# Kernel tuning notes

Hardware: AMD Instinct MI355X
Metric: run time of the kernel (lower is better)

The kernel has to match this reference:

```python
import jax, jax.numpy as jnp
import numpy as np
from jax import lax

B, C, H, W = 2, 64, 384, 384
WS = 8; NH = 4; HD = C // NH; S = WS * WS  # 64 tokens per window
EPS = 1e-5


def setup_inputs() -> dict:
    key = jax.random.key(0)
    ks = jax.random.split(key, 16)
    def n(k, shape, s=0.02):
        return jax.random.normal(k, shape, jnp.float32) * s
    return {
        "x": jax.random.normal(ks[0], (B, C, H, W), jnp.float32),
        "norm1_w": jnp.ones((C,), jnp.float32), "norm1_b": jnp.zeros((C,), jnp.float32),
        "qkv_w": n(ks[1], (3 * C, C)), "qkv_b": jnp.zeros((3 * C,), jnp.float32),
        "pos_bias": n(ks[2], (1, S, NH, NH), 0.01),  # faithful: bias over (tokens, heads, heads)
        "out_w": n(ks[3], (C, C)), "out_b": jnp.zeros((C,), jnp.float32),
        "convp_w": n(ks[4], (C, C)), "convp_b": jnp.zeros((C,), jnp.float32),
        "pw1_w": n(ks[5], (C, C, 1)), "pw1_b": jnp.zeros((C,), jnp.float32),
        "dw1_w": n(ks[6], (C, 1, 3)), "dw1_b": jnp.zeros((C,), jnp.float32),
        "tok_w": n(ks[7], (C, C)), "tok_b": jnp.zeros((C,), jnp.float32),
        "norm2_w": jnp.ones((C,), jnp.float32), "norm2_b": jnp.zeros((C,), jnp.float32),
        "leff_pw_w": n(ks[8], (C, C, 1, 1)),
        "leff_dw_w": n(ks[9], (C, 1, 3, 3)), "leff_dw_b": jnp.zeros((C,), jnp.float32),
        "fc1_w": n(ks[10], (4 * C, C)), "fc1_b": jnp.zeros((4 * C,), jnp.float32),
        "fc2_w": n(ks[11], (C, 4 * C)), "fc2_b": jnp.zeros((C,), jnp.float32),
    }


def _ln_c(x, w, b):
    # channel-wise LayerNorm (Restormer 'WithBias') on (B,C,H,W), biased variance
    mu = x.mean(axis=1, keepdims=True)
    var = ((x - mu) ** 2).mean(axis=1, keepdims=True)
    return (x - mu) / jnp.sqrt(var + EPS) * w[None, :, None, None] + b[None, :, None, None]


def _lin(x, w, b):
    return x @ w.T + b


def _win_part(x):
    # (B,C,H,W) -> (B*nw, S, C); H,W divisible by WS so pad is a no-op
    b = x.shape[0]
    x = x.reshape(b, C, H // WS, WS, W // WS, WS)
    return x.transpose(0, 2, 4, 3, 5, 1).reshape(-1, S, C)


def _win_merge(wins):
    b = wins.shape[0] // ((H // WS) * (W // WS))
    x = wins.reshape(b, H // WS, W // WS, WS, WS, C)
    return x.transpose(0, 5, 1, 3, 2, 4).reshape(b, C, H, W)


def _remsa(xw, qkv_w, qkv_b, pos_bias, out_w, out_b, convp_w, convp_b,
           pw1_w, pw1_b, dw1_w, dw1_b, tok_w, tok_b):
    bw = xw.shape[0]
    qkv = _lin(xw, qkv_w, qkv_b).reshape(bw, S, NH, 3 * HD)
    q, k, v = jnp.split(qkv, 3, axis=-1)  # each (bw, S, NH, HD)
    # Faithful to source: NO head transpose -> attention mixes across the heads axis
    scores = jnp.einsum('bshd,bsgd->bshg', q, k) * (HD ** -0.5) + pos_bias  # (bw,S,NH,NH)
    attn = jax.nn.softmax(scores, axis=-1)
    ao = jnp.einsum('bshg,bsgd->bshd', attn, v).reshape(bw, S, C)
    ao = _lin(ao, out_w, out_b)
    # convolutional branch
    xc = _lin(xw, convp_w, convp_b).transpose(0, 2, 1)  # (bw, C, S)
    xc = jnp.einsum('bcs,oc->bos', xc, pw1_w[:, :, 0]) + pw1_b[None, :, None]  # 1x1 conv1d
    xc = lax.conv_general_dilated(xc, dw1_w, (1,), 'SAME', feature_group_count=C,
                                  dimension_numbers=('NCH', 'OIH', 'NCH')) + dw1_b[None, :, None]
    xc = _lin(xc.transpose(0, 2, 1), tok_w, tok_b)
    return ao + xc


def _leff(x, pw_w, dw_w, dw_b, fc1_w, fc1_b, fc2_w, fc2_b):
    b = x.shape[0]
    y = lax.conv_general_dilated(x, pw_w, (1, 1), 'SAME',
                                 dimension_numbers=('NCHW', 'OIHW', 'NCHW'))  # 1x1, no bias
    y = lax.conv_general_dilated(y, dw_w, (1, 1), 'SAME', feature_group_count=C,
                                 dimension_numbers=('NCHW', 'OIHW', 'NCHW')) + dw_b[None, :, None, None]
    y = y.transpose(0, 2, 3, 1).reshape(b, H * W, C)
    y = jax.nn.gelu(_lin(y, fc1_w, fc1_b), approximate=False)
    y = _lin(y, fc2_w, fc2_b)
    return y.reshape(b, H, W, C).transpose(0, 3, 1, 2)


def reference(x, norm1_w, norm1_b, qkv_w, qkv_b, pos_bias, out_w, out_b,
              convp_w, convp_b, pw1_w, pw1_b, dw1_w, dw1_b, tok_w, tok_b,
              norm2_w, norm2_b, leff_pw_w, leff_dw_w, leff_dw_b,
              fc1_w, fc1_b, fc2_w, fc2_b):
    xw = _win_part(_ln_c(x, norm1_w, norm1_b))
    r = _win_merge(_remsa(xw, qkv_w, qkv_b, pos_bias, out_w, out_b, convp_w, convp_b,
                          pw1_w, pw1_b, dw1_w, dw1_b, tok_w, tok_b))
    x = x + r
    x = x + _leff(_ln_c(x, norm2_w, norm2_b), leff_pw_w, leff_dw_w, leff_dw_b,
                  fc1_w, fc1_b, fc2_w, fc2_b)
    return x
```

## Files before the change

### kernel.cpp

```cpp
#include <hip/hip_runtime.h>
#include <hip/hip_bf16.h>
#include <math.h>

#define Bn 2
#define Cc 64
#define Hh 384
#define Ww 384
#define HW (Hh*Ww)
#define Tt (Bn*HW)

using f32x4  = __attribute__((ext_vector_type(4))) float;
using bf16x8 = __attribute__((ext_vector_type(8))) short;


__device__ __forceinline__ unsigned short f2bf_u(float f) {
  return __builtin_bit_cast(unsigned short, __float2bfloat16(f));
}
__device__ __forceinline__ float bf2f(unsigned short u) {
  union { unsigned u; float f; } v; v.u = ((unsigned)u) << 16;
  return v.f;
}
__device__ __forceinline__ float gelu_exact(float v) {
  return 0.5f * v * (1.0f + erff(v * 0.70710678118654752f));
}

__device__ __forceinline__ void stage_wtile(char* dst, const float* __restrict__ g, int rs, int tid) {
#pragma unroll
  for (int half = 0; half < 2; ++half) {
    int q = tid + half * 256;
    int row = q >> 3, ks = q & 7;
    const float* gp = g + (long)row * rs + ks * 8;
    float4 a = *(const float4*)gp;
    float4 b = *(const float4*)(gp + 4);
    bf16x8 o;
    o[0] = (short)f2bf_u(a.x); o[1] = (short)f2bf_u(a.y);
    o[2] = (short)f2bf_u(a.z); o[3] = (short)f2bf_u(a.w);
    o[4] = (short)f2bf_u(b.x); o[5] = (short)f2bf_u(b.y);
    o[6] = (short)f2bf_u(b.z); o[7] = (short)f2bf_u(b.w);
    *(bf16x8*)(dst + row * 128 + ((ks * 16) ^ ((row & 7) << 4))) = o;
  }
}

__device__ __forceinline__ void mfma64(const char* sA, const char* sB, int wid, int lane, f32x4 acc[4]) {
  const int r = lane & 15, kq = lane >> 4;
#pragma unroll
  for (int kh = 0; kh < 2; ++kh) {
    const int arow = wid * 16 + r;
    bf16x8 af = *(const bf16x8*)(sA + arow * 128 + ((kh * 64 + kq * 16) ^ ((arow & 7) << 4)));
#pragma unroll
    for (int nt = 0; nt < 4; ++nt) {
      const int brow = nt * 16 + r;
      bf16x8 bfv = *(const bf16x8*)(sB + brow * 128 + ((kh * 64 + kq * 16) ^ ((brow & 7) << 4)));
      acc[nt] = __builtin_amdgcn_mfma_f32_16x16x32_bf16(af, bfv, acc[nt], 0, 0, 0);
    }
  }
}


__global__ __launch_bounds__(512, 4) void kA(
    const float* __restrict__ x, unsigned short* __restrict__ x1g, unsigned short* __restrict__ yg,
    const float* __restrict__ n1w, const float* __restrict__ n1b,
    const float* __restrict__ qkvw, const float* __restrict__ qkvb,
    const float* __restrict__ posb,
    const float* __restrict__ outw, const float* __restrict__ outb,
    const float* __restrict__ cpw, const float* __restrict__ cpb,
    const float* __restrict__ pw1w, const float* __restrict__ pw1b,
    const float* __restrict__ dw1w, const float* __restrict__ dw1b,
    const float* __restrict__ tokw, const float* __restrict__ tokb,
    const float* __restrict__ n2w, const float* __restrict__ n2b,
    const float* __restrict__ lpw) {
  __shared__ char sX[16384];
  __shared__ char sW0[8192];
  __shared__ char sW1[8192];
  __shared__ char sQ[49152];

  const int tid = threadIdx.x;
  const int lane = tid & 63, wid = tid >> 6;
  const int fr = lane & 15, kq = lane >> 4;
  const int rtok = wid * 16 + fr;
  const int c0own = kq * 16;
  const int iy = wid, ix = fr;
  const int blk = blockIdx.x;
  const int b = blk / 1152;
  const int rr = blk - b * 1152;
  const int wy = rr / 24, wxp = rr - (rr / 24) * 24;
  const int h0 = wy * 8, w0 = wxp * 16;
  const long ibase = (long)b * HW;

  float4 wr0, wr1;
  const int wrow = tid >> 3, wc0 = (tid & 7) * 8;
  auto WLOAD = [&](const float* g) {
    const float* p = g + (long)wrow * 64 + wc0;
    wr0 = *(const float4*)p; wr1 = *(const float4*)(p + 4);
  };
  auto WSTORE = [&](char* dst) {
    bf16x8 o;
    o[0]=(short)f2bf_u(wr0.x); o[1]=(short)f2bf_u(wr0.y); o[2]=(short)f2bf_u(wr0.z); o[3]=(short)f2bf_u(wr0.w);
    o[4]=(short)f2bf_u(wr1.x); o[5]=(short)f2bf_u(wr1.y); o[6]=(short)f2bf_u(wr1.z); o[7]=(short)f2bf_u(wr1.w);
    *(bf16x8*)(dst + wrow * 128 + ((2 * wc0) ^ ((wrow & 7) << 4))) = o;
  };

  WLOAD(cpw);
  const float* xb = x + ((long)(b * 64 + c0own)) * HW + (long)(h0 + iy) * Ww + (w0 + ix);
  float vx[16]; float s0 = 0.f, s1 = 0.f;
#pragma unroll
  for (int k = 0; k < 16; ++k) {
    float v = xb[(long)k * HW];
    vx[k] = v; s0 += v; s1 += v * v;
  }
  s0 += __shfl_xor(s0, 16); s0 += __shfl_xor(s0, 32);
  s1 += __shfl_xor(s1, 16); s1 += __shfl_xor(s1, 32);
  {
    float m = s0 * (1.f / 64.f);
    float ri = rsqrtf(s1 * (1.f / 64.f) - m * m + 1e-5f);
    const int swz = (rtok & 7) << 4;
#pragma unroll
    for (int q8 = 0; q8 < 2; ++q8) {
      bf16x8 o;
#pragma unroll
      for (int j = 0; j < 8; ++j) {
        int c = c0own + q8 * 8 + j;
        o[j] = (short)f2bf_u((vx[q8 * 8 + j] - m) * ri * n1w[c] + n1b[c]);
      }
      *(bf16x8*)(sX + rtok * 128 + ((c0own * 2 + q8 * 16) ^ swz)) = o;
    }
  }
  WSTORE(sW0); WLOAD(pw1w);
  __syncthreads();

  f32x4 acc[4], res[4];
  auto ZERO = [&](f32x4 a[4]) {
#pragma unroll
    for (int nt = 0; nt < 4; ++nt) a[nt] = (f32x4){0.f, 0.f, 0.f, 0.f};
  };
  auto GEMM = [&](const char* A, const char* W, f32x4 a[4]) {
#pragma unroll
    for (int kh = 0; kh < 2; ++kh) {
      const int arow = wid * 16 + fr;
      bf16x8 af = *(const bf16x8*)(A + arow * 128 + ((kh * 64 + kq * 16) ^ ((arow & 7) << 4)));
#pragma unroll
      for (int nt = 0; nt < 4; ++nt) {
        const int brow = nt * 16 + fr;
        bf16x8 bv = *(const bf16x8*)(W + brow * 128 + ((kh * 64 + kq * 16) ^ ((brow & 7) << 4)));
        a[nt] = __builtin_amdgcn_mfma_f32_16x16x32_bf16(af, bv, a[nt], 0, 0, 0);
      }
    }
  };
  auto EPI = [&](char* dst, f32x4 a[4], const float* bias) {
    const int rb = wid * 16 + kq * 4;
#pragma unroll
    for (int nt = 0; nt < 4; ++nt) {
      const int col = nt * 16 + fr;
      const float bv = bias[col];
#pragma unroll
      for (int reg = 0; reg < 4; ++reg) {
        const int row = rb + reg;
        *(unsigned short*)(dst + row * 128 + ((2 * col) ^ ((row & 7) << 4))) = f2bf_u(a[nt][reg] + bv);
      }
    }
  };
  char* t0 = sQ; char* t1 = sQ + 16384; char* t2 = sQ + 32768;
  float* sQf = (float*)sQ;

  ZERO(acc); GEMM(sX, sW0, acc); EPI(t0, acc, cpb);
  WSTORE(sW1); WLOAD(tokw);
  __syncthreads();
  ZERO(acc); GEMM(t0, sW1, acc); EPI(t1, acc, pw1b);
  WSTORE(sW0); WLOAD(qkvw);
  __syncthreads();
  {
    const int c = tid & 63, tq = tid >> 6;
    const int wl = tq >> 2, chunk = tq & 3;
    float wv0 = dw1w[c * 3], wv1 = dw1w[c * 3 + 1], wv2 = dw1w[c * 3 + 2], bia = dw1b[c];
#pragma unroll
    for (int k = 0; k < 16; ++k) {
      int s = chunk * 16 + k;
      int r0 = ((s >> 3) << 4) + wl * 8 + (s & 7);
      float v = bia + bf2f(*(const unsigned short*)(t1 + r0 * 128 + ((2 * c) ^ ((r0 & 7) << 4)))) * wv1;
      if (s > 0) {
        int rm = (((s - 1) >> 3) << 4) + wl * 8 + ((s - 1) & 7);
        v += bf2f(*(const unsigned short*)(t1 + rm * 128 + ((2 * c) ^ ((rm & 7) << 4)))) * wv0;
      }
      if (s < 63) {
        int rp = (((s + 1) >> 3) << 4) + wl * 8 + ((s + 1) & 7);
        v += bf2f(*(const unsigned short*)(t1 + rp * 128 + ((2 * c) ^ ((rp & 7) << 4)))) * wv2;
      }
      *(unsigned short*)(t0 + r0 * 128 + ((2 * c) ^ ((r0 & 7) << 4))) = f2bf_u(v);
    }
  }
  WSTORE(sW1); WLOAD(qkvw + 4096);
  __syncthreads();
  ZERO(res); GEMM(t0, sW0, res);
  __syncthreads();
  ZERO(acc); GEMM(sX, sW1, acc); EPI(t0, acc, qkvb);
  WSTORE(sW0); WLOAD(qkvw + 8192);
  __syncthreads();
  ZERO(acc); GEMM(sX, sW0, acc); EPI(t1, acc, qkvb + 64);
  WSTORE(sW1); WLOAD(outw);
  __syncthreads();
  ZERO(acc); GEMM(sX, sW1, acc); EPI(t2, acc, qkvb + 128);
  WSTORE(sW0); WLOAD(lpw);
  __syncthreads();
  {
    const int r = rtok;
    const int h = kq;
    const int s = ((r >> 4) << 3) + (r & 7);
    const int swz = (r & 7) << 4;
    auto LD16 = [&](int gcol, float* o) {
      const char* base = sQ + ((gcol >> 6) * 16384) + r * 128;
      int c0 = (gcol & 63) * 2;
      bf16x8 u = *(const bf16x8*)(base + (c0 ^ swz));
      bf16x8 w2_ = *(const bf16x8*)(base + ((c0 + 16) ^ swz));
#pragma unroll
      for (int j = 0; j < 8; ++j) {
        o[j] = bf2f((unsigned short)u[j]); o[8 + j] = bf2f((unsigned short)w2_[j]);
      }
    };
    float q0[16];
    LD16(48 * h, q0);
    float sc[4];
#pragma unroll
    for (int g = 0; g < 4; ++g) {
      float kk[16]; LD16(48 * g + 16, kk);
      float a = 0.f;
#pragma unroll
      for (int d = 0; d < 16; ++d) a += q0[d] * kk[d];
      sc[g] = a * 0.25f + posb[s * 16 + h * 4 + g];
    }
    float m = fmaxf(fmaxf(sc[0], sc[1]), fmaxf(sc[2], sc[3]));
    float e[4]; float tsum = 0.f;
#pragma unroll
    for (int g = 0; g < 4; ++g) { e[g] = __expf(sc[g] - m); tsum += e[g]; }
    float inv = 1.f / tsum;
    float ao[16];
#pragma unroll
    for (int d = 0; d < 16; ++d) ao[d] = 0.f;
#pragma unroll
    for (int g = 0; g < 4; ++g) {
      float vv[16]; LD16(48 * g + 32, vv);
#pragma unroll
      for (int d = 0; d < 16; ++d) ao[d] += e[g] * vv[d];
    }
    bf16x8 o1, o2;
#pragma unroll
    for (int j = 0; j < 8; ++j) { o1[j] = (short)f2bf_u(ao[j] * inv); o2[j] = (short)f2bf_u(ao[8 + j] * inv); }
    *(bf16x8*)(sX + r * 128 + ((h * 32) ^ swz)) = o1;
    *(bf16x8*)(sX + r * 128 + ((h * 32 + 16) ^ swz)) = o2;
  }
  WSTORE(sW1);
  __syncthreads();
  GEMM(sX, sW0, res);
  {
    const int rb = wid * 16 + kq * 4;
#pragma unroll
    for (int nt = 0; nt < 4; ++nt) {
      const int col = nt * 16 + fr;
      const float ob = outb[col] + tokb[col];
#pragma unroll
      for (int reg = 0; reg < 4; ++reg)
        sQf[(rb + reg) * 67 + col] = res[nt][reg] + ob;
    }
  }
  __syncthreads();
  {
    float ss0 = 0.f, ss1 = 0.f;
#pragma unroll
    for (int k = 0; k < 16; ++k) {
      float v = sQf[rtok * 67 + c0own + k] + vx[k];
      vx[k] = v; ss0 += v; ss1 += v * v;
    }
    ss0 += __shfl_xor(ss0, 16); ss0 += __shfl_xor(ss0, 32);
    ss1 += __shfl_xor(ss1, 16); ss1 += __shfl_xor(ss1, 32);
    float m = ss0 * (1.f / 64.f);
    float ri = rsqrtf(ss1 * (1.f / 64.f) - m * m + 1e-5f);
    const int swz = (rtok & 7) << 4;
    long t = ibase + (long)(h0 + iy) * Ww + (w0 + ix);
#pragma unroll
    for (int q8 = 0; q8 < 2; ++q8) {
      bf16x8 xo, no;
#pragma unroll
      for (int j = 0; j < 8; ++j) {
        int c = c0own + q8 * 8 + j;
        float v = vx[q8 * 8 + j];
        xo[j] = (short)f2bf_u(v);
        no[j] = (short)f2bf_u((v - m) * ri * n2w[c] + n2b[c]);
      }
      *(bf16x8*)((char*)x1g + t * 128 + (c0own + q8 * 8) * 2) = xo;
      *(bf16x8*)(sX + rtok * 128 + ((c0own * 2 + q8 * 16) ^ swz)) = no;
    }
  }
  __syncthreads();
  ZERO(acc); GEMM(sX, sW1, acc);
  {
    const int rb = wid * 16 + kq * 4;
#pragma unroll
    for (int nt = 0; nt < 4; ++nt) {
      const int col = nt * 16 + fr;
#pragma unroll
      for (int reg = 0; reg < 4; ++reg)
        sQf[(rb + reg) * 67 + col] = acc[nt][reg];
    }
  }
  __syncthreads();
  {
    long t = ibase + (long)(h0 + iy) * Ww + (w0 + ix);
#pragma unroll
    for (int q8 = 0; q8 < 2; ++q8) {
      bf16x8 o;
#pragma unroll
      for (int j = 0; j < 8; ++j)
        o[j] = (short)f2bf_u(sQf[rtok * 67 + c0own + q8 * 8 + j]);
      *(bf16x8*)((char*)yg + t * 128 + (c0own + q8 * 8) * 2) = o;
    }
  }
}


__global__ __launch_bounds__(256, 3) void kB(
    const unsigned short* __restrict__ yg, const unsigned short* __restrict__ x1g,
    float* __restrict__ out,
    const float* __restrict__ ldw, const float* __restrict__ ldb,
    const float* __restrict__ f1w, const float* __restrict__ f1b,
    const float* __restrict__ f2w, const float* __restrict__ f2b) {
  __shared__ char sZ0[8192];
  __shared__ char sZ1[8192];
  __shared__ char U[33792];
  __shared__ float wtab[640];

  const int tid = threadIdx.x;
  const int lane = tid & 63, wid = tid >> 6;
  const int bid = blockIdx.x;
  const int b = bid / 1152;
  const int r2 = bid - b * 1152;
  const int hp = r2 / 6, wseg = r2 - (r2 / 6) * 6;
  const int h0 = hp * 2, w0 = wseg * 64;
  const long ibase = (long)b * HW;
  const int cbase = lane & 15;
  const int rbase = wid * 16 + (lane >> 4) * 4;

  unsigned short x1r[2][4][4];
#pragma unroll
  for (int t = 0; t < 2; ++t) {
    const long p0t = ibase + (long)(h0 + t) * Ww + w0;
#pragma unroll
    for (int nt = 0; nt < 4; ++nt) {
      int col = nt * 16 + cbase;
#pragma unroll
      for (int reg = 0; reg < 4; ++reg)
        x1r[t][nt][reg] = x1g[(p0t + rbase + reg) * 64 + col];
    }
  }

#pragma unroll
  for (int it = 0; it < 3; ++it) {
    int idx = it * 256 + tid;
    if (idx < 576) wtab[idx] = ldw[(idx & 63) * 9 + (idx >> 6)];
    else if (idx < 640) wtab[idx] = ldb[idx - 576];
  }

  for (int it = 0; it < 9; ++it) {
    int idx = it * 256 + tid;
    if (idx >= 2112) break;
    int hr = idx / 528;
    int rq = idx - hr * 528;
    int px = rq >> 3, c8 = rq & 7;
    int h = h0 - 1 + hr, w = w0 - 1 + px;
    uint4 v = make_uint4(0, 0, 0, 0);
    if (h >= 0 && h < Hh && w >= 0 && w < Ww) {
      long t = ibase + (long)h * Ww + w;
      v = *(const uint4*)((const char*)yg + t * 128 + c8 * 16);
    }
    int X = hr * 66 + px;
    *(uint4*)(U + X * 128 + ((c8 * 16) ^ ((X & 7) << 4))) = v;
  }
  __syncthreads();

  {
    const int c8 = tid & 7, c0 = c8 * 8;
#pragma unroll
    for (int it = 0; it < 4; ++it) {
      int task = it * 256 + tid;
      int r = task >> 9;
      int px = (task >> 3) & 63;
      float a8[8];
#pragma unroll
      for (int j = 0; j < 8; ++j) a8[j] = wtab[576 + c0 + j];
#pragma unroll
      for (int dy = 0; dy < 3; ++dy)
#pragma unroll
        for (int dx = 0; dx < 3; ++dx) {
          int X = (r + dy) * 66 + px + dx;
          bf16x8 v = *(const bf16x8*)(U + X * 128 + ((c8 * 16) ^ ((X & 7) << 4)));
          const float* wk = wtab + (dy * 3 + dx) * 64 + c0;
#pragma unroll
          for (int j = 0; j < 8; ++j) a8[j] += bf2f((unsigned short)v[j]) * wk[j];
        }
      char* sZ = r ? sZ1 : sZ0;
      bf16x8 o;
#pragma unroll
      for (int j = 0; j < 8; ++j) o[j] = (short)f2bf_u(a8[j]);
      *(bf16x8*)(sZ + px * 128 + ((c8 * 16) ^ ((px & 7) << 4))) = o;
    }
  }
  __syncthreads();

  char* sW  = U;
  char* sH0 = U + 8192;
  char* sH1 = U + 16384;
  f32x4 res0[4], res1[4];
#pragma unroll
  for (int nt = 0; nt < 4; ++nt) { res0[nt] = (f32x4){0.f,0.f,0.f,0.f}; res1[nt] = (f32x4){0.f,0.f,0.f,0.f}; }

  for (int jc = 0; jc < 4; ++jc) {
    stage_wtile(sW, f1w + jc * 4096, 64, tid);
    __syncthreads();
#pragma unroll
    for (int t = 0; t < 2; ++t) {
      f32x4 acc[4];
#pragma unroll
      for (int nt = 0; nt < 4; ++nt) acc[nt] = (f32x4){0.f,0.f,0.f,0.f};
      mfma64(t ? sZ1 : sZ0, sW, wid, lane, acc);
      char* sH = t ? sH1 : sH0;
#pragma unroll
      for (int nt = 0; nt < 4; ++nt) {
        const int col = nt * 16 + cbase;
        const float bv = f1b[jc * 64 + col];
#pragma unroll
        for (int reg = 0; reg < 4; ++reg) {
          const int row = rbase + reg;
          *(unsigned short*)(sH + row * 128 + ((col * 2) ^ ((row & 7) << 4))) =
              f2bf_u(gelu_exact(acc[nt][reg] + bv));
        }
      }
    }
    __syncthreads();
    stage_wtile(sW, f2w + jc * 64, 256, tid);
    __syncthreads();
    mfma64(sH0, sW, wid, lane, res0);
    mfma64(sH1, sW, wid, lane, res1);
    __syncthreads();
  }

  float* sO = (float*)U;
#pragma unroll
  for (int t = 0; t < 2; ++t) {
    const f32x4* res = t ? res1 : res0;
#pragma unroll
    for (int nt = 0; nt < 4; ++nt) {
      const int col = nt * 16 + cbase;
      const float bv = f2b[col];
#pragma unroll
      for (int reg = 0; reg < 4; ++reg) {
        const int row = rbase + reg;
        sO[row * 65 + col] = res[nt][reg] + bv + bf2f(x1r[t][nt][reg]);
      }
    }
    __syncthreads();
#pragma unroll
    for (int it = 0; it < 16; ++it) {
      int c = it * 4 + (tid >> 6);
      int wo = tid & 63;
      out[(((long)(b * Cc + c)) * Hh + (h0 + t)) * Ww + w0 + wo] = sO[wo * 65 + c];
    }
    __syncthreads();
  }
}


extern "C" void kernel_launch(void* const* d_in, const int* in_sizes, int n_in,
                              void* d_out, int out_size, void* d_ws, size_t ws_size,
                              hipStream_t stream) {
  const float* x    = (const float*)d_in[0];
  const float* n1w  = (const float*)d_in[1];
  const float* n1b  = (const float*)d_in[2];
  const float* qkvw = (const float*)d_in[3];
  const float* qkvb = (const float*)d_in[4];
  const float* posb = (const float*)d_in[5];
  const float* outw = (const float*)d_in[6];
  const float* outb = (const float*)d_in[7];
  const float* cpw  = (const float*)d_in[8];
  const float* cpb  = (const float*)d_in[9];
  const float* pw1w = (const float*)d_in[10];
  const float* pw1b = (const float*)d_in[11];
  const float* dw1w = (const float*)d_in[12];
  const float* dw1b = (const float*)d_in[13];
  const float* tokw = (const float*)d_in[14];
  const float* tokb = (const float*)d_in[15];
  const float* n2w  = (const float*)d_in[16];
  const float* n2b  = (const float*)d_in[17];
  const float* lpw  = (const float*)d_in[18];
  const float* ldw  = (const float*)d_in[19];
  const float* ldb  = (const float*)d_in[20];
  const float* f1w  = (const float*)d_in[21];
  const float* f1b  = (const float*)d_in[22];
  const float* f2w  = (const float*)d_in[23];
  const float* f2b  = (const float*)d_in[24];
  float* out = (float*)d_out;

  unsigned short* x1 = (unsigned short*)d_ws;
  unsigned short* y  = x1 + (size_t)Tt * 64;

  kA<<<dim3(2304), dim3(512), 0, stream>>>(x, x1, y, n1w, n1b, qkvw, qkvb, posb,
                                           outw, outb, cpw, cpb, pw1w, pw1b,
                                           dw1w, dw1b, tokw, tokb, n2w, n2b, lpw);
  kB<<<dim3(2304), dim3(256), 0, stream>>>(y, x1, out, ldw, ldb, f1w, f1b, f2w, f2b);
}
```

Baseline: 189.9 us.

## Double kB block to 512 threads, one wave group per output row

Kernel kB now launches 512 threads per block instead of 256, and each group of four waves owns one of the two image rows. The MLP MFMA work, the depthwise staging loops and the weight-tile staging are split across the larger block, so each wave does half the previous work. The final output transpose also writes both rows after a single barrier. This is meant to cut per-wave serial work and add latency hiding per block, at the cost of fewer resident blocks per CU (launch bounds 512,2) and wider barriers.

```diff
diff --git a/kernel.cpp b/kernel.cpp
--- a/kernel.cpp
+++ b/kernel.cpp
@@ -24,36 +24,17 @@
   return 0.5f * v * (1.0f + erff(v * 0.70710678118654752f));
 }
 
-__device__ __forceinline__ void stage_wtile(char* dst, const float* __restrict__ g, int rs, int tid) {
-#pragma unroll
-  for (int half = 0; half < 2; ++half) {
-    int q = tid + half * 256;
-    int row = q >> 3, ks = q & 7;
-    const float* gp = g + (long)row * rs + ks * 8;
-    float4 a = *(const float4*)gp;
-    float4 b = *(const float4*)(gp + 4);
-    bf16x8 o;
-    o[0] = (short)f2bf_u(a.x); o[1] = (short)f2bf_u(a.y);
-    o[2] = (short)f2bf_u(a.z); o[3] = (short)f2bf_u(a.w);
-    o[4] = (short)f2bf_u(b.x); o[5] = (short)f2bf_u(b.y);
-    o[6] = (short)f2bf_u(b.z); o[7] = (short)f2bf_u(b.w);
-    *(bf16x8*)(dst + row * 128 + ((ks * 16) ^ ((row & 7) << 4))) = o;
-  }
-}
-
-__device__ __forceinline__ void mfma64(const char* sA, const char* sB, int wid, int lane, f32x4 acc[4]) {
-  const int r = lane & 15, kq = lane >> 4;
-#pragma unroll
-  for (int kh = 0; kh < 2; ++kh) {
-    const int arow = wid * 16 + r;
-    bf16x8 af = *(const bf16x8*)(sA + arow * 128 + ((kh * 64 + kq * 16) ^ ((arow & 7) << 4)));
-#pragma unroll
-    for (int nt = 0; nt < 4; ++nt) {
-      const int brow = nt * 16 + r;
-      bf16x8 bfv = *(const bf16x8*)(sB + brow * 128 + ((kh * 64 + kq * 16) ^ ((brow & 7) << 4)));
-      acc[nt] = __builtin_amdgcn_mfma_f32_16x16x32_bf16(af, bfv, acc[nt], 0, 0, 0);
-    }
-  }
+__device__ __forceinline__ void stage_wtile512(char* dst, const float* __restrict__ g, int rs, int tid) {
+  const int row = tid >> 3, ks = tid & 7;
+  const float* gp = g + (long)row * rs + ks * 8;
+  float4 a = *(const float4*)gp;
+  float4 b = *(const float4*)(gp + 4);
+  bf16x8 o;
+  o[0] = (short)f2bf_u(a.x); o[1] = (short)f2bf_u(a.y);
+  o[2] = (short)f2bf_u(a.z); o[3] = (short)f2bf_u(a.w);
+  o[4] = (short)f2bf_u(b.x); o[5] = (short)f2bf_u(b.y);
+  o[6] = (short)f2bf_u(b.z); o[7] = (short)f2bf_u(b.w);
+  *(bf16x8*)(dst + row * 128 + ((ks * 16) ^ ((row & 7) << 4))) = o;
 }
 
 
@@ -316,7 +297,7 @@
 }
 
 
-__global__ __launch_bounds__(256, 3) void kB(
+__global__ __launch_bounds__(512, 2) void kB(
     const unsigned short* __restrict__ yg, const unsigned short* __restrict__ x1g,
     float* __restrict__ out,
     const float* __restrict__ ldw, const float* __restrict__ ldb,
@@ -329,37 +310,39 @@
 
   const int tid = threadIdx.x;
   const int lane = tid & 63, wid = tid >> 6;
+  const int fr = lane & 15, kq = lane >> 4;
+  const int t_own = wid >> 2;
+  const int wv = wid & 3;
   const int bid = blockIdx.x;
   const int b = bid / 1152;
   const int r2 = bid - b * 1152;
   const int hp = r2 / 6, wseg = r2 - (r2 / 6) * 6;
   const int h0 = hp * 2, w0 = wseg * 64;
   const long ibase = (long)b * HW;
-  const int cbase = lane & 15;
-  const int rbase = wid * 16 + (lane >> 4) * 4;
-
-  unsigned short x1r[2][4][4];
-#pragma unroll
-  for (int t = 0; t < 2; ++t) {
-    const long p0t = ibase + (long)(h0 + t) * Ww + w0;
+  const int cbase = fr;
+  const int rbase = wv * 16 + kq * 4;
+
+  unsigned short x1r[4][4];
+  {
+    const long p0t = ibase + (long)(h0 + t_own) * Ww + w0;
 #pragma unroll
     for (int nt = 0; nt < 4; ++nt) {
       int col = nt * 16 + cbase;
 #pragma unroll
       for (int reg = 0; reg < 4; ++reg)
-        x1r[t][nt][reg] = x1g[(p0t + rbase + reg) * 64 + col];
-    }
-  }
-
-#pragma unroll
-  for (int it = 0; it < 3; ++it) {
-    int idx = it * 256 + tid;
+        x1r[nt][reg] = x1g[(p0t + rbase + reg) * 64 + col];
+    }
+  }
+
+#pragma unroll
+  for (int it = 0; it < 2; ++it) {
+    int idx = it * 512 + tid;
     if (idx < 576) wtab[idx] = ldw[(idx & 63) * 9 + (idx >> 6)];
     else if (idx < 640) wtab[idx] = ldb[idx - 576];
   }
 
-  for (int it = 0; it < 9; ++it) {
-    int idx = it * 256 + tid;
+  for (int it = 0; it < 5; ++it) {
+    int idx = it * 512 + tid;
     if (idx >= 2112) break;
     int hr = idx / 528;
     int rq = idx - hr * 528;
@@ -376,10 +359,11 @@
   __syncthreads();
 
   {
-    const int c8 = tid & 7, c0 = c8 * 8;
-#pragma unroll
-    for (int it = 0; it < 4; ++it) {
-      int task = it * 256 + tid;
+    const int c8l = tid & 7;
+    const int c0 = c8l * 8;
+#pragma unroll
+    for (int it = 0; it < 2; ++it) {
+      int task = it * 512 + tid;
       int r = task >> 9;
       int px = (task >> 3) & 63;
       float a8[8];
@@ -390,7 +374,7 @@
 #pragma unroll
         for (int dx = 0; dx < 3; ++dx) {
           int X = (r + dy) * 66 + px + dx;
-          bf16x8 v = *(const bf16x8*)(U + X * 128 + ((c8 * 16) ^ ((X & 7) << 4)));
+          bf16x8 v = *(const bf16x8*)(U + X * 128 + ((c8l * 16) ^ ((X & 7) << 4)));
           const float* wk = wtab + (dy * 3 + dx) * 64 + c0;
 #pragma unroll
           for (int j = 0; j < 8; ++j) a8[j] += bf2f((unsigned short)v[j]) * wk[j];
@@ -399,7 +383,7 @@
       bf16x8 o;
 #pragma unroll
       for (int j = 0; j < 8; ++j) o[j] = (short)f2bf_u(a8[j]);
-      *(bf16x8*)(sZ + px * 128 + ((c8 * 16) ^ ((px & 7) << 4))) = o;
+      *(bf16x8*)(sZ + px * 128 + ((c8l * 16) ^ ((px & 7) << 4))) = o;
     }
   }
   __syncthreads();
@@ -407,20 +391,30 @@
   char* sW  = U;
   char* sH0 = U + 8192;
   char* sH1 = U + 16384;
-  f32x4 res0[4], res1[4];
-#pragma unroll
-  for (int nt = 0; nt < 4; ++nt) { res0[nt] = (f32x4){0.f,0.f,0.f,0.f}; res1[nt] = (f32x4){0.f,0.f,0.f,0.f}; }
+  char* sZt = t_own ? sZ1 : sZ0;
+  char* sHt = t_own ? sH1 : sH0;
+  f32x4 res[4];
+#pragma unroll
+  for (int nt = 0; nt < 4; ++nt) res[nt] = (f32x4){0.f, 0.f, 0.f, 0.f};
 
   for (int jc = 0; jc < 4; ++jc) {
-    stage_wtile(sW, f1w + jc * 4096, 64, tid);
+    stage_wtile512(sW, f1w + jc * 4096, 64, tid);
     __syncthreads();
-#pragma unroll
-    for (int t = 0; t < 2; ++t) {
+    {
       f32x4 acc[4];
 #pragma unroll
-      for (int nt = 0; nt < 4; ++nt) acc[nt] = (f32x4){0.f,0.f,0.f,0.f};
-      mfma64(t ? sZ1 : sZ0, sW, wid, lane, acc);
-      char* sH = t ? sH1 : sH0;
+      for (int nt = 0; nt < 4; ++nt) acc[nt] = (f32x4){0.f, 0.f, 0.f, 0.f};
+#pragma unroll
+      for (int kh = 0; kh < 2; ++kh) {
+        const int arow = wv * 16 + fr;
+        bf16x8 af = *(const bf16x8*)(sZt + arow * 128 + ((kh * 64 + kq * 16) ^ ((arow & 7) << 4)));
+#pragma unroll
+        for (int nt = 0; nt < 4; ++nt) {
+          const int brow = nt * 16 + fr;
+          bf16x8 bv = *(const bf16x8*)(sW + brow * 128 + ((kh * 64 + kq * 16) ^ ((brow & 7) << 4)));
+          acc[nt] = __builtin_amdgcn_mfma_f32_16x16x32_bf16(af, bv, acc[nt], 0, 0, 0);
+        }
+      }
 #pragma unroll
       for (int nt = 0; nt < 4; ++nt) {
         const int col = nt * 16 + cbase;
@@ -428,41 +422,49 @@
 #pragma unroll
         for (int reg = 0; reg < 4; ++reg) {
           const int row = rbase + reg;
-          *(unsigned short*)(sH + row * 128 + ((col * 2) ^ ((row & 7) << 4))) =
+          *(unsigned short*)(sHt + row * 128 + ((col * 2) ^ ((row & 7) << 4))) =
               f2bf_u(gelu_exact(acc[nt][reg] + bv));
         }
       }
     }
     __syncthreads();
-    stage_wtile(sW, f2w + jc * 64, 256, tid);
+    stage_wtile512(sW, f2w + jc * 64, 256, tid);
     __syncthreads();
-    mfma64(sH0, sW, wid, lane, res0);
-    mfma64(sH1, sW, wid, lane, res1);
+#pragma unroll
+    for (int kh = 0; kh < 2; ++kh) {
+      const int arow = wv * 16 + fr;
+      bf16x8 af = *(const bf16x8*)(sHt + arow * 128 + ((kh * 64 + kq * 16) ^ ((arow & 7) << 4)));
+#pragma unroll
+      for (int nt = 0; nt < 4; ++nt) {
+        const int brow = nt * 16 + fr;
+        bf16x8 bv = *(const bf16x8*)(sW + brow * 128 + ((kh * 64 + kq * 16) ^ ((brow & 7) << 4)));
+        res[nt] = __builtin_amdgcn_mfma_f32_16x16x32_bf16(af, bv, res[nt], 0, 0, 0);
+      }
+    }
     __syncthreads();
   }
 
   float* sO = (float*)U;
 #pragma unroll
-  for (int t = 0; t < 2; ++t) {
-    const f32x4* res = t ? res1 : res0;
-#pragma unroll
-    for (int nt = 0; nt < 4; ++nt) {
-      const int col = nt * 16 + cbase;
-      const float bv = f2b[col];
-#pragma unroll
-      for (int reg = 0; reg < 4; ++reg) {
-        const int row = rbase + reg;
-        sO[row * 65 + col] = res[nt][reg] + bv + bf2f(x1r[t][nt][reg]);
-      }
-    }
-    __syncthreads();
+  for (int nt = 0; nt < 4; ++nt) {
+    const int col = nt * 16 + cbase;
+    const float bv = f2b[col];
+#pragma unroll
+    for (int reg = 0; reg < 4; ++reg) {
+      const int row = rbase + reg;
+      sO[t_own * 4160 + row * 65 + col] = res[nt][reg] + bv + bf2f(x1r[nt][reg]);
+    }
+  }
+  __syncthreads();
+  {
+    const int t = tid >> 8;
+    const int tt = tid & 255;
 #pragma unroll
     for (int it = 0; it < 16; ++it) {
-      int c = it * 4 + (tid >> 6);
-      int wo = tid & 63;
-      out[(((long)(b * Cc + c)) * Hh + (h0 + t)) * Ww + w0 + wo] = sO[wo * 65 + c];
-    }
-    __syncthreads();
+      int c = it * 4 + (tt >> 6);
+      int wo = tt & 63;
+      out[(((long)(b * Cc + c)) * Hh + (h0 + t)) * Ww + w0 + wo] = sO[t * 4160 + wo * 65 + c];
+    }
   }
 }
 
@@ -503,5 +505,5 @@
   kA<<<dim3(2304), dim3(512), 0, stream>>>(x, x1, y, n1w, n1b, qkvw, qkvb, posb,
                                            outw, outb, cpw, cpb, pw1w, pw1b,
                                            dw1w, dw1b, tokw, tokb, n2w, n2b, lpw);
-  kB<<<dim3(2304), dim3(256), 0, stream>>>(y, x1, out, ldw, ldb, f1w, f1b, f2w, f2b);
-}
+  kB<<<dim3(2304), dim3(512), 0, stream>>>(y, x1, out, ldw, ldb, f1w, f1b, f2w, f2b);
+}
```

Result: faster. 174.9 us (-7.9%).
